# Performance work log

Measured on AMD Instinct MI355X. Metric: run time of the kernel, lower is better.

Reference implementation:

```python
import math
import jax, jax.numpy as jnp
import numpy as np

NUM_SUPERPIXELS = 256
COMPACTNESS = 10.0
NUM_ITERATIONS = 5


def _cdist(a, b):
    # Euclidean pairwise distance: a [B,N,C], b [B,K,C] -> [B,N,K]
    a2 = jnp.sum(a * a, axis=-1)[:, :, None]
    b2 = jnp.sum(b * b, axis=-1)[:, None, :]
    ab = jnp.einsum('bnc,bkc->bnk', a, b)
    return jnp.sqrt(jnp.maximum(a2 + b2 - 2.0 * ab, 1e-12))


def setup_inputs() -> dict:
    key = jax.random.key(0)
    x = jax.random.normal(key, (4, 200, 128, 128), dtype=jnp.float32)
    return {"x": x}


def reference(x):
    B, C, H, W = x.shape
    N = H * W

    # --- initialize_centers (grid of seed pixels, taken from x[0]) ---
    grid_h = int(math.sqrt(NUM_SUPERPIXELS * H / W))
    grid_w = NUM_SUPERPIXELS // grid_h
    K = grid_h * grid_w
    h_step, w_step = H // grid_h, W // grid_w
    h_idx = jnp.arange(h_step // 2, H, h_step)[:grid_h]
    w_idx = jnp.arange(w_step // 2, W, w_step)[:grid_w]
    gy, gx = jnp.meshgrid(h_idx, w_idx, indexing='ij')
    init_spatial = jnp.stack([gy.flatten(), gx.flatten()], axis=1).astype(jnp.float32)  # [K,2]
    flat_idx = gy.flatten() * W + gx.flatten()  # [K]

    # --- pixel coordinates ---
    yg, xg = jnp.meshgrid(jnp.arange(H), jnp.arange(W), indexing='ij')
    pix = jnp.stack([yg.flatten(), xg.flatten()], axis=1).astype(jnp.float32)  # [N,2]
    pix_b = jnp.broadcast_to(pix[None], (B, N, 2))

    x_flat = jnp.transpose(x, (0, 2, 3, 1)).reshape(B, N, C)  # [B,N,C]
    centers_spectral = jnp.broadcast_to(x_flat[0][flat_idx][None], (B, K, C))
    centers_spatial = jnp.broadcast_to(init_spatial[None], (B, K, 2))

    S = math.sqrt(H * W / NUM_SUPERPIXELS)
    Q = None
    for _ in range(NUM_ITERATIONS):
        D = _cdist(x_flat, centers_spectral) + (COMPACTNESS / S) * _cdist(pix_b, centers_spatial)
        Q = jax.nn.softmax(-D, axis=-1)  # [B,N,K]
        mass = jnp.sum(Q, axis=1)[:, :, None] + 1e-06  # [B,K,1]
        centers_spectral = jnp.einsum('bnk,bnc->bkc', Q, x_flat) / mass
        centers_spatial = jnp.einsum('bnk,bnc->bkc', Q, pix_b) / mass
    return Q, centers_spectral
```

## Files before the change

### kernel.cpp

```cpp
#include <hip/hip_runtime.h>
#include <math.h>

#define B 4
#define C 200
#define H 128
#define W 128
#define N 16384
#define K 256
#define ITERS 5
#define FACT 1.25f
#define NT 32
#define NTM 128
#define CPAD 208
#define CP2  224

typedef __attribute__((ext_vector_type(8))) __bf16 bf16x8;
typedef __attribute__((ext_vector_type(4))) __bf16 bf16x4;
typedef __attribute__((ext_vector_type(4))) float f32x4;

#define OFF_A2    0
#define OFF_CS    (OFF_A2 + B*N)
#define OFF_CSPAT (OFF_CS + B*K*C)
#define OFF_B2    (OFF_CSPAT + B*K*2)
#define OFF_SACC  (OFF_B2 + B*K)
#define OFF_MACC  (OFF_SACC + B*K*C)
#define OFF_SPACC (OFF_MACC + B*K)
#define OFF_CST   (OFF_SPACC + B*K*2)
#define CST_SZ    (B*C*K)
#define OFF_PART  (OFF_CST + CST_SZ)
#define PART_SZ   (B*NT*CPAD*K)
#define OFF_MPART (OFF_PART + PART_SZ)
#define MPART_SZ  (B*NTM*3*K)
#define WS_NEED   ((size_t)(OFF_MPART + MPART_SZ) * 4)
#define OFF_XBF   (OFF_MPART + MPART_SZ)
#define XBF_SZF   (B*N*CP2/2)
#define OFF_CSBF  (OFF_XBF + XBF_SZF)
#define CSBF_SZF  (B*K*CP2/2)
#define WS_NEED2  ((size_t)(OFF_CSBF + CSBF_SZF) * 4)
#define OFF_QTB   (OFF_CSBF + CSBF_SZF)
#define QTB_SZF   (B*K*N/2)
#define OFF_XB2   (OFF_QTB + QTB_SZF)
#define XB2_SZF   (B*CPAD*N/2)
#define WS_NEED3  ((size_t)(OFF_XB2 + XB2_SZF) * 4)

__global__ void k_init(const float* __restrict__ x, float* __restrict__ cs,
                       __bf16* __restrict__ csbf, float* __restrict__ cspat,
                       int fast) {
  int k = blockIdx.x, c = threadIdx.x;
  int i = k >> 4, j = k & 15;
  int sn = (4 + 8*i)*W + (4 + 8*j);
  if (c < C) {
    float v = x[(size_t)c*N + sn];
    for (int b = 0; b < B; ++b) {
      cs[((size_t)(b*K + k))*C + c] = v;
      if (fast) csbf[((size_t)(b*K + k))*CP2 + c] = (__bf16)v;
    }
  } else if (fast && c < CP2) {
    for (int b = 0; b < B; ++b)
      csbf[((size_t)(b*K + k))*CP2 + c] = (__bf16)0.f;
  }
  if (c == 0) {
    for (int b = 0; b < B; ++b) {
      cspat[(b*K + k)*2 + 0] = (float)(4 + 8*i);
      cspat[(b*K + k)*2 + 1] = (float)(4 + 8*j);
    }
  }
}

__global__ __launch_bounds__(256) void k_prep(const float* __restrict__ x,
                                              __bf16* __restrict__ xbf) {
  __shared__ float xt[32*64];
  int bid = blockIdx.x;
  int b  = bid >> 8;
  int n0 = (bid & 255) << 6;
  int tid = threadIdx.x;
  const float* xb = x + (size_t)b*C*N;
  __bf16* xo = xbf + ((size_t)b*N + n0)*CP2;
  for (int t = 0; t < 7; ++t) {
    int cc0 = t*32;
    __syncthreads();
    #pragma unroll
    for (int pass = 0; pass < 2; ++pass) {
      int f = pass*256 + tid;
      int ci = f >> 4, nq = f & 15;
      float4 v = make_float4(0.f, 0.f, 0.f, 0.f);
      if (cc0 + ci < C) v = *(const float4*)&xb[(size_t)(cc0 + ci)*N + n0 + nq*4];
      *(float4*)&xt[ci*64 + nq*4] = v;
    }
    __syncthreads();
    {
      int n = tid & 63, cg8 = (tid >> 6) * 8;
      bf16x8 pk;
      #pragma unroll
      for (int i = 0; i < 8; ++i) pk[i] = (__bf16)xt[(cg8 + i)*64 + n];
      *(bf16x8*)&xo[(size_t)n*CP2 + cc0 + cg8] = pk;
    }
  }
}

__global__ __launch_bounds__(256) void k_prep2(const float* __restrict__ x,
                                               __bf16* __restrict__ xbf2) {
  int g = blockIdx.x * 256 + threadIdx.x;
  int per_b = CPAD * (N/8);
  int b = g / per_b;
  int rem = g - b*per_b;
  int c = rem / (N/8);
  int n = (rem - c*(N/8)) * 8;
  bf16x8 pk;
  if (c < C) {
    const float* src = &x[((size_t)b*C + c)*N + n];
    float4 v0 = *(const float4*)&src[0];
    float4 v1 = *(const float4*)&src[4];
    pk[0]=(__bf16)v0.x; pk[1]=(__bf16)v0.y; pk[2]=(__bf16)v0.z; pk[3]=(__bf16)v0.w;
    pk[4]=(__bf16)v1.x; pk[5]=(__bf16)v1.y; pk[6]=(__bf16)v1.z; pk[7]=(__bf16)v1.w;
  } else {
    #pragma unroll
    for (int i = 0; i < 8; ++i) pk[i] = (__bf16)0.f;
  }
  *(bf16x8*)&xbf2[((size_t)b*CPAD + c)*N + n] = pk;
}

__global__ void k_a2(const float* __restrict__ x, float* __restrict__ a2) {
  int b = blockIdx.x >> 6;
  int n = ((blockIdx.x & 63) << 8) + threadIdx.x;
  const float* xp = x + (size_t)b*C*N + n;
  float s = 0.f;
  #pragma unroll 8
  for (int c = 0; c < C; ++c) { float v = xp[(size_t)c*N]; s += v*v; }
  a2[b*N + n] = s;
}

__global__ void k_b2(const float* __restrict__ cs, float* __restrict__ b2) {
  int bk = blockIdx.x;
  const float* p = cs + (size_t)bk*C;
  float s = 0.f;
  for (int c = threadIdx.x; c < C; c += 64) { float v = p[c]; s += v*v; }
  for (int off = 32; off > 0; off >>= 1) s += __shfl_down(s, off);
  if (threadIdx.x == 0) b2[bk] = s;
}

__global__ __launch_bounds__(512, 2) void k_assign2(
    const __bf16* __restrict__ xbf, const __bf16* __restrict__ csbf,
    const float* __restrict__ cspat, const float* __restrict__ b2,
    const float* __restrict__ a2, float* __restrict__ Q,
    __bf16* __restrict__ qtb, int wq) {
  __shared__ float b2s[K], cys[K], cxs[K];
  __shared__ float a2s[128];
  __shared__ float redw[8*128];
  __shared__ float redf[128];

  int b   = blockIdx.x >> 7;
  int n0  = (blockIdx.x & 127) << 7;
  int tid = threadIdx.x;
  int lane = tid & 63;
  int lr = lane & 15;
  int lg = lane >> 4;
  int w  = tid >> 6;

  if (tid < K) {
    b2s[tid] = b2[b*K + tid];
    cys[tid] = cspat[(b*K + tid)*2 + 0];
    cxs[tid] = cspat[(b*K + tid)*2 + 1];
  }
  if (tid < 128) a2s[tid] = a2[b*N + n0 + tid];
  __syncthreads();

  f32x4 acc[16];
  #pragma unroll
  for (int i = 0; i < 16; ++i) acc[i] = (f32x4){0.f, 0.f, 0.f, 0.f};

  const __bf16* cb = csbf + ((size_t)b*K + (size_t)(w*32 + lr))*CP2;
  const __bf16* xb = xbf + ((size_t)(b*N + n0 + lr))*CP2;

  for (int t = 0; t < 7; ++t) {
    int cc = t*32 + lg*8;
    bf16x8 b0 = *(const bf16x8*)&cb[cc];
    bf16x8 b1 = *(const bf16x8*)&cb[(size_t)16*CP2 + cc];
    #pragma unroll
    for (int nt = 0; nt < 8; ++nt) {
      bf16x8 av = *(const bf16x8*)&xb[(size_t)(nt*16)*CP2 + cc];
      acc[nt*2+0] = __builtin_amdgcn_mfma_f32_16x16x32_bf16(av, b0, acc[nt*2+0], 0, 0, 0);
      acc[nt*2+1] = __builtin_amdgcn_mfma_f32_16x16x32_bf16(av, b1, acc[nt*2+1], 0, 0, 0);
    }
  }

  float py = (float)(n0 >> 7);
  int k0 = w*32 + lr, k1 = k0 + 16;
  float b2v0 = b2s[k0], b2v1 = b2s[k1];
  float cx0 = cxs[k0], cx1 = cxs[k1];
  float dy0 = py - cys[k0], dy1 = py - cys[k1];
  float dyy0 = dy0*dy0, dyy1 = dy1*dy1;

  float mArr[32];
  #pragma unroll
  for (int nt = 0; nt < 8; ++nt) {
    #pragma unroll
    for (int r = 0; r < 4; ++r) {
      int pix = nt*16 + lg*4 + r;
      float a2v = a2s[pix];
      float pxv = (float)pix;
      float dx0 = pxv - cx0, dx1 = pxv - cx1;
      float d0 = sqrtf(fmaxf(a2v + b2v0 - 2.f*acc[nt*2+0][r], 1e-12f))
               + FACT*sqrtf(fmaxf(dyy0 + dx0*dx0, 1e-12f));
      float d1 = sqrtf(fmaxf(a2v + b2v1 - 2.f*acc[nt*2+1][r], 1e-12f))
               + FACT*sqrtf(fmaxf(dyy1 + dx1*dx1, 1e-12f));
      float e0 = __expf(-d0);
      float e1 = __expf(-d1);
      acc[nt*2+0][r] = e0;
      acc[nt*2+1][r] = e1;
      float s = e0 + e1;
      s += __shfl_xor(s, 1);
      s += __shfl_xor(s, 2);
      s += __shfl_xor(s, 4);
      s += __shfl_xor(s, 8);
      mArr[nt*4+r] = s;
    }
  }
  if (lr == 0) {
    #pragma unroll
    for (int nt = 0; nt < 8; ++nt)
      #pragma unroll
      for (int r = 0; r < 4; ++r)
        redw[w*128 + nt*16 + lg*4 + r] = mArr[nt*4+r];
  }
  __syncthreads();
  if (tid < 128) {
    float s = redw[tid];
    #pragma unroll
    for (int g = 1; g < 8; ++g) s += redw[g*128 + tid];
    redf[tid] = 1.f / s;
  }
  __syncthreads();
  float* Qb = Q + ((size_t)(b*N + n0))*K;
  __bf16* qt0 = qtb + ((size_t)b*K + k0)*N + n0;
  __bf16* qt1 = qtb + ((size_t)b*K + k1)*N + n0;
  #pragma unroll
  for (int nt = 0; nt < 8; ++nt) {
    bf16x4 p0, p1;
    #pragma unroll
    for (int r = 0; r < 4; ++r) {
      int pix = nt*16 + lg*4 + r;
      float inv = redf[pix];
      float f0 = acc[nt*2+0][r] * inv;
      float f1 = acc[nt*2+1][r] * inv;
      Qb[(size_t)pix*K + k0] = f0;
      Qb[(size_t)pix*K + k1] = f1;
      p0[r] = (__bf16)f0;
      p1[r] = (__bf16)f1;
    }
    if (wq) {
      *(bf16x4*)&qt0[nt*16 + lg*4] = p0;
      *(bf16x4*)&qt1[nt*16 + lg*4] = p1;
    }
  }
}

__global__ __launch_bounds__(512, 2) void k_assign(
    const float* __restrict__ x, const float* __restrict__ cs,
    const float* __restrict__ cspat, const float* __restrict__ b2,
    const float* __restrict__ a2, float* __restrict__ Q) {
  __shared__ __bf16 cs_lds[K*40];
  __shared__ __bf16 x_lds[128*40];
  __shared__ float b2s[K], cys[K], cxs[K];
  __shared__ float a2s[128];
  __shared__ float redw[8*128];
  __shared__ float redf[128];

  int b   = blockIdx.x >> 7;
  int n0  = (blockIdx.x & 127) << 7;
  int tid = threadIdx.x;
  int lane = tid & 63;
  int lr = lane & 15;
  int lg = lane >> 4;
  int w  = tid >> 6;

  if (tid < K) {
    b2s[tid] = b2[b*K + tid];
    cys[tid] = cspat[(b*K + tid)*2 + 0];
    cxs[tid] = cspat[(b*K + tid)*2 + 1];
  }
  if (tid < 128) a2s[tid] = a2[b*N + n0 + tid];

  f32x4 acc[16];
  #pragma unroll
  for (int i = 0; i < 16; ++i) acc[i] = (f32x4){0.f, 0.f, 0.f, 0.f};

  const float* xb = x + (size_t)b*C*N;
  const float* cb = cs + (size_t)b*K*C;

  for (int t = 0; t < 7; ++t) {
    int cc0 = t * 32;
    __syncthreads();
    #pragma unroll
    for (int pass = 0; pass < 4; ++pass) {
      int f = pass*512 + tid;
      int k = f >> 3, c4 = (f & 7) * 4;
      float4 v = make_float4(0.f, 0.f, 0.f, 0.f);
      if (cc0 + c4 < 200) v = *(const float4*)&cb[(size_t)k*C + cc0 + c4];
      __bf16* d = &cs_lds[k*40 + c4];
      d[0] = (__bf16)v.x; d[1] = (__bf16)v.y;
      d[2] = (__bf16)v.z; d[3] = (__bf16)v.w;
    }
    #pragma unroll
    for (int pass = 0; pass < 8; ++pass) {
      int idx = pass*512 + tid;
      int ci = idx >> 7, p = idx & 127;
      float xv = (cc0 + ci < 200) ? xb[(size_t)(cc0 + ci)*N + n0 + p] : 0.f;
      x_lds[p*40 + ci] = (__bf16)xv;
    }
    __syncthreads();
    const __bf16* bbase = &cs_lds[(w*32 + lr)*40 + lg*8];
    bf16x8 b0 = *(const bf16x8*)bbase;
    bf16x8 b1 = *(const bf16x8*)(bbase + 16*40);
    const __bf16* abase = &x_lds[lr*40 + lg*8];
    #pragma unroll
    for (int nt = 0; nt < 8; ++nt) {
      bf16x8 av = *(const bf16x8*)(abase + nt*16*40);
      acc[nt*2+0] = __builtin_amdgcn_mfma_f32_16x16x32_bf16(av, b0, acc[nt*2+0], 0, 0, 0);
      acc[nt*2+1] = __builtin_amdgcn_mfma_f32_16x16x32_bf16(av, b1, acc[nt*2+1], 0, 0, 0);
    }
  }

  float py = (float)(n0 >> 7);
  float mArr[32];
  #pragma unroll
  for (int nt = 0; nt < 8; ++nt) {
    #pragma unroll
    for (int r = 0; r < 4; ++r) {
      int pix = nt*16 + lg*4 + r;
      float a2v = a2s[pix];
      float pxv = (float)pix;
      float dmin = 1e30f;
      #pragma unroll
      for (int j = 0; j < 2; ++j) {
        int k = w*32 + j*16 + lr;
        float ab = acc[nt*2+j][r];
        float dy = py - cys[k];
        float dx = pxv - cxs[k];
        float d = sqrtf(fmaxf(a2v + b2s[k] - 2.f*ab, 1e-12f))
                + FACT*sqrtf(fmaxf(dy*dy + dx*dx, 1e-12f));
        acc[nt*2+j][r] = d;
        dmin = fminf(dmin, d);
      }
      mArr[nt*4+r] = dmin;
    }
  }
  #pragma unroll
  for (int i = 0; i < 32; ++i) {
    float m = mArr[i];
    m = fminf(m, __shfl_xor(m, 1));
    m = fminf(m, __shfl_xor(m, 2));
    m = fminf(m, __shfl_xor(m, 4));
    m = fminf(m, __shfl_xor(m, 8));
    mArr[i] = m;
  }
  if (lr == 0) {
    #pragma unroll
    for (int nt = 0; nt < 8; ++nt)
      #pragma unroll
      for (int r = 0; r < 4; ++r)
        redw[w*128 + nt*16 + lg*4 + r] = mArr[nt*4+r];
  }
  __syncthreads();
  if (tid < 128) {
    float m = redw[tid];
    #pragma unroll
    for (int g = 1; g < 8; ++g) m = fminf(m, redw[g*128 + tid]);
    redf[tid] = m;
  }
  __syncthreads();
  #pragma unroll
  for (int nt = 0; nt < 8; ++nt) {
    #pragma unroll
    for (int r = 0; r < 4; ++r) {
      int pix = nt*16 + lg*4 + r;
      float mnv = redf[pix];
      float s = 0.f;
      #pragma unroll
      for (int j = 0; j < 2; ++j) {
        float e = __expf(mnv - acc[nt*2+j][r]);
        acc[nt*2+j][r] = e;
        s += e;
      }
      s += __shfl_xor(s, 1);
      s += __shfl_xor(s, 2);
      s += __shfl_xor(s, 4);
      s += __shfl_xor(s, 8);
      mArr[nt*4+r] = s;
    }
  }
  if (lr == 0) {
    #pragma unroll
    for (int nt = 0; nt < 8; ++nt)
      #pragma unroll
      for (int r = 0; r < 4; ++r)
        redw[w*128 + nt*16 + lg*4 + r] = mArr[nt*4+r];
  }
  __syncthreads();
  if (tid < 128) {
    float s = redw[tid];
    #pragma unroll
    for (int g = 1; g < 8; ++g) s += redw[g*128 + tid];
    redf[tid] = 1.f / s;
  }
  __syncthreads();
  float* Qb = Q + ((size_t)(b*N + n0))*K;
  #pragma unroll
  for (int nt = 0; nt < 8; ++nt) {
    #pragma unroll
    for (int r = 0; r < 4; ++r) {
      int pix = nt*16 + lg*4 + r;
      float inv = redf[pix];
      #pragma unroll
      for (int j = 0; j < 2; ++j) {
        int k = w*32 + j*16 + lr;
        Qb[(size_t)pix*K + k] = acc[nt*2+j][r] * inv;
      }
    }
  }
}

__global__ __launch_bounds__(256) void k_update5(
    const __bf16* __restrict__ qtb, const __bf16* __restrict__ xbf2,
    float* __restrict__ part) {
  int bid = blockIdx.x;
  int b   = bid >> 7;
  int rem = bid & 127;
  int cg  = rem >> 5;
  int nt  = rem & 31;
  int tid = threadIdx.x;
  int lane = tid & 63, lr = lane & 15, lg = lane >> 4;
  int w   = tid >> 6;
  int c0  = cg * 64;

  f32x4 acc[16];
  #pragma unroll
  for (int i = 0; i < 16; ++i) acc[i] = (f32x4){0.f, 0.f, 0.f, 0.f};

  const __bf16* qb = qtb + ((size_t)b*K + (size_t)(w*64 + lr))*N;
  int cr0 = c0 + lr;
  int cr1 = min(c0 + 16 + lr, CPAD - 1);
  int cr2 = min(c0 + 32 + lr, CPAD - 1);
  int cr3 = min(c0 + 48 + lr, CPAD - 1);
  const __bf16* xb0 = xbf2 + ((size_t)b*CPAD + cr0)*N;
  const __bf16* xb1 = xbf2 + ((size_t)b*CPAD + cr1)*N;
  const __bf16* xb2 = xbf2 + ((size_t)b*CPAD + cr2)*N;
  const __bf16* xb3 = xbf2 + ((size_t)b*CPAD + cr3)*N;

  for (int ch = 0; ch < 16; ++ch) {
    int nb = nt*512 + ch*32 + lg*8;
    bf16x8 A0 = *(const bf16x8*)&qb[nb];
    bf16x8 A1 = *(const bf16x8*)&qb[(size_t)16*N + nb];
    bf16x8 A2 = *(const bf16x8*)&qb[(size_t)32*N + nb];
    bf16x8 A3 = *(const bf16x8*)&qb[(size_t)48*N + nb];
    bf16x8 B0 = *(const bf16x8*)&xb0[nb];
    bf16x8 B1 = *(const bf16x8*)&xb1[nb];
    bf16x8 B2 = *(const bf16x8*)&xb2[nb];
    bf16x8 B3 = *(const bf16x8*)&xb3[nb];
    acc[0]  = __builtin_amdgcn_mfma_f32_16x16x32_bf16(A0, B0, acc[0], 0, 0, 0);
    acc[1]  = __builtin_amdgcn_mfma_f32_16x16x32_bf16(A0, B1, acc[1], 0, 0, 0);
    acc[2]  = __builtin_amdgcn_mfma_f32_16x16x32_bf16(A0, B2, acc[2], 0, 0, 0);
    acc[3]  = __builtin_amdgcn_mfma_f32_16x16x32_bf16(A0, B3, acc[3], 0, 0, 0);
    acc[4]  = __builtin_amdgcn_mfma_f32_16x16x32_bf16(A1, B0, acc[4], 0, 0, 0);
    acc[5]  = __builtin_amdgcn_mfma_f32_16x16x32_bf16(A1, B1, acc[5], 0, 0, 0);
    acc[6]  = __builtin_amdgcn_mfma_f32_16x16x32_bf16(A1, B2, acc[6], 0, 0, 0);
    acc[7]  = __builtin_amdgcn_mfma_f32_16x16x32_bf16(A1, B3, acc[7], 0, 0, 0);
    acc[8]  = __builtin_amdgcn_mfma_f32_16x16x32_bf16(A2, B0, acc[8], 0, 0, 0);
    acc[9]  = __builtin_amdgcn_mfma_f32_16x16x32_bf16(A2, B1, acc[9], 0, 0, 0);
    acc[10] = __builtin_amdgcn_mfma_f32_16x16x32_bf16(A2, B2, acc[10], 0, 0, 0);
    acc[11] = __builtin_amdgcn_mfma_f32_16x16x32_bf16(A2, B3, acc[11], 0, 0, 0);
    acc[12] = __builtin_amdgcn_mfma_f32_16x16x32_bf16(A3, B0, acc[12], 0, 0, 0);
    acc[13] = __builtin_amdgcn_mfma_f32_16x16x32_bf16(A3, B1, acc[13], 0, 0, 0);
    acc[14] = __builtin_amdgcn_mfma_f32_16x16x32_bf16(A3, B2, acc[14], 0, 0, 0);
    acc[15] = __builtin_amdgcn_mfma_f32_16x16x32_bf16(A3, B3, acc[15], 0, 0, 0);
  }

  float* pp = part + (size_t)(b*NT + nt) * CPAD * K;
  #pragma unroll
  for (int t = 0; t < 4; ++t) {
    #pragma unroll
    for (int u = 0; u < 4; ++u) {
      int c = c0 + u*16 + lr;
      if (c < CPAD) {
        int k = w*64 + t*16 + lg*4;
        *(f32x4*)&pp[(size_t)c*K + k] = acc[t*4+u];
      }
    }
  }
}

__global__ __launch_bounds__(256) void k_update4(
    const float* __restrict__ x, const float* __restrict__ Q,
    float* __restrict__ part) {
  __shared__ float  q32[32*256];
  __shared__ __bf16 qbf[256*40];
  __shared__ __bf16 xbf[64*40];
  int bid = blockIdx.x;
  int b   = bid >> 7;
  int rem = bid & 127;
  int cg  = rem >> 5;
  int nt  = rem & 31;
  int tid = threadIdx.x;
  int lane = tid & 63, lr = lane & 15, lg = lane >> 4;
  int w   = tid >> 6;
  int c0  = cg * 64;

  f32x4 acc[16];
  #pragma unroll
  for (int i = 0; i < 16; ++i) acc[i] = (f32x4){0.f, 0.f, 0.f, 0.f};

  const float* Qb = Q + (size_t)b*N*K;
  const float* xb = x + (size_t)b*C*N;

  for (int ch = 0; ch < 16; ++ch) {
    int nb = nt*512 + ch*32;
    __syncthreads();
    #pragma unroll
    for (int pass = 0; pass < 8; ++pass) {
      int f = pass*256 + tid;
      int n = f >> 6, k4 = f & 63;
      *(float4*)&q32[n*256 + k4*4] =
          *(const float4*)&Qb[(size_t)(nb + n)*K + k4*4];
    }
    #pragma unroll
    for (int pass = 0; pass < 2; ++pass) {
      int f = pass*256 + tid;
      int c = f >> 3, n4 = f & 7;
      int cc = c0 + c;
      float4 v = make_float4(0.f, 0.f, 0.f, 0.f);
      if (cc < 200) v = *(const float4*)&xb[(size_t)cc*N + nb + n4*4];
      __bf16* d = &xbf[c*40 + n4*4];
      d[0] = (__bf16)v.x; d[1] = (__bf16)v.y;
      d[2] = (__bf16)v.z; d[3] = (__bf16)v.w;
    }
    __syncthreads();
    {
      #pragma unroll
      for (int g = 0; g < 4; ++g) {
        bf16x8 pk;
        #pragma unroll
        for (int i = 0; i < 8; ++i)
          pk[i] = (__bf16)q32[(g*8 + i)*256 + tid];
        *(bf16x8*)&qbf[tid*40 + g*8] = pk;
      }
    }
    __syncthreads();
    const __bf16* abase = &qbf[(w*64 + lr)*40 + lg*8];
    const __bf16* bbase = &xbf[lr*40 + lg*8];
    bf16x8 A0 = *(const bf16x8*)(abase);
    bf16x8 A1 = *(const bf16x8*)(abase + 16*40);
    bf16x8 A2 = *(const bf16x8*)(abase + 32*40);
    bf16x8 A3 = *(const bf16x8*)(abase + 48*40);
    bf16x8 B0 = *(const bf16x8*)(bbase);
    bf16x8 B1 = *(const bf16x8*)(bbase + 16*40);
    bf16x8 B2 = *(const bf16x8*)(bbase + 32*40);
    bf16x8 B3 = *(const bf16x8*)(bbase + 48*40);
    acc[0]  = __builtin_amdgcn_mfma_f32_16x16x32_bf16(A0, B0, acc[0], 0, 0, 0);
    acc[1]  = __builtin_amdgcn_mfma_f32_16x16x32_bf16(A0, B1, acc[1], 0, 0, 0);
    acc[2]  = __builtin_amdgcn_mfma_f32_16x16x32_bf16(A0, B2, acc[2], 0, 0, 0);
    acc[3]  = __builtin_amdgcn_mfma_f32_16x16x32_bf16(A0, B3, acc[3], 0, 0, 0);
    acc[4]  = __builtin_amdgcn_mfma_f32_16x16x32_bf16(A1, B0, acc[4], 0, 0, 0);
    acc[5]  = __builtin_amdgcn_mfma_f32_16x16x32_bf16(A1, B1, acc[5], 0, 0, 0);
    acc[6]  = __builtin_amdgcn_mfma_f32_16x16x32_bf16(A1, B2, acc[6], 0, 0, 0);
    acc[7]  = __builtin_amdgcn_mfma_f32_16x16x32_bf16(A1, B3, acc[7], 0, 0, 0);
    acc[8]  = __builtin_amdgcn_mfma_f32_16x16x32_bf16(A2, B0, acc[8], 0, 0, 0);
    acc[9]  = __builtin_amdgcn_mfma_f32_16x16x32_bf16(A2, B1, acc[9], 0, 0, 0);
    acc[10] = __builtin_amdgcn_mfma_f32_16x16x32_bf16(A2, B2, acc[10], 0, 0, 0);
    acc[11] = __builtin_amdgcn_mfma_f32_16x16x32_bf16(A2, B3, acc[11], 0, 0, 0);
    acc[12] = __builtin_amdgcn_mfma_f32_16x16x32_bf16(A3, B0, acc[12], 0, 0, 0);
    acc[13] = __builtin_amdgcn_mfma_f32_16x16x32_bf16(A3, B1, acc[13], 0, 0, 0);
    acc[14] = __builtin_amdgcn_mfma_f32_16x16x32_bf16(A3, B2, acc[14], 0, 0, 0);
    acc[15] = __builtin_amdgcn_mfma_f32_16x16x32_bf16(A3, B3, acc[15], 0, 0, 0);
  }

  float* pp = part + (size_t)(b*NT + nt) * CPAD * K;
  #pragma unroll
  for (int t = 0; t < 4; ++t) {
    #pragma unroll
    for (int u = 0; u < 4; ++u) {
      int c = c0 + u*16 + lr;
      if (c < CPAD) {
        int k = w*64 + t*16 + lg*4;
        *(f32x4*)&pp[(size_t)c*K + k] = acc[t*4+u];
      }
    }
  }
}

__global__ __launch_bounds__(256) void k_mass(
    const float* __restrict__ Q, float* __restrict__ mpart) {
  int bid = blockIdx.x;
  int b = bid >> 7, nt = bid & 127;
  int tid = threadIdx.x;
  const float* Qb = Q + (size_t)b*N*K;
  int nbase = nt * 128;
  float mass = 0.f, sy = 0.f, sx = 0.f;
  for (int nn = 0; nn < 128; nn += 8) {
    float qv[8];
    #pragma unroll
    for (int j = 0; j < 8; ++j)
      qv[j] = Qb[(size_t)(nbase + nn + j)*K + tid];
    #pragma unroll
    for (int j = 0; j < 8; ++j) {
      int n = nbase + nn + j;
      mass += qv[j];
      sy += qv[j] * (float)(n >> 7);
      sx += qv[j] * (float)(n & 127);
    }
  }
  float* mp = mpart + (size_t)(b*NTM + nt) * 3 * K;
  mp[tid]       = mass;
  mp[K + tid]   = sy;
  mp[2*K + tid] = sx;
}

__global__ __launch_bounds__(256) void k_reduce(
    const float* __restrict__ part, const float* __restrict__ mpart,
    float* __restrict__ sacc, float* __restrict__ macc,
    float* __restrict__ spacc) {
  int bid = blockIdx.x;
  int b = bid / 200;
  int c = bid % 200;
  int tid = threadIdx.x;
  float s = 0.f;
  for (int nt = 0; nt < NT; ++nt)
    s += part[((size_t)(b*NT + nt)*CPAD + c)*K + tid];
  sacc[(size_t)(b*K + tid)*C + c] = s;
  if (c == 0) {
    float m = 0.f, yy = 0.f, xx = 0.f;
    for (int nt = 0; nt < NTM; ++nt) {
      const float* mp = mpart + (size_t)(b*NTM + nt) * 3 * K;
      m  += mp[tid];
      yy += mp[K + tid];
      xx += mp[2*K + tid];
    }
    macc[b*K + tid] = m;
    spacc[(b*K + tid)*2 + 0] = yy;
    spacc[(b*K + tid)*2 + 1] = xx;
  }
}

__global__ __launch_bounds__(256, 2) void k_update(
    const float* __restrict__ x, const float* __restrict__ Q,
    float* __restrict__ sacc, float* __restrict__ macc,
    float* __restrict__ spacc) {
  __shared__ float x_lds[32*28];
  int bid = blockIdx.x;
  int b = bid >> 9;
  int rest = bid & 511;
  int ct = rest >> 6;
  int nt = rest & 63;
  int tid = threadIdx.x;
  int c0 = ct * 25;

  float acc[25];
  #pragma unroll
  for (int c = 0; c < 25; ++c) acc[c] = 0.f;
  float mass = 0.f, sy = 0.f, sx = 0.f;

  const float* xb = x + (size_t)b*C*N + (size_t)c0*N;
  const float* Qb = Q + (size_t)b*N*K;

  for (int ch = 0; ch < 8; ++ch) {
    int nb = nt*256 + ch*32;
    __syncthreads();
    #pragma unroll
    for (int pass = 0; pass < 4; ++pass) {
      int idx = pass*256 + tid;
      if (idx < 800) {
        int ci = idx >> 5, nn = idx & 31;
        x_lds[nn*28 + ci] = xb[(size_t)ci*N + nb + nn];
      }
    }
    __syncthreads();
    float py  = (float)(nb >> 7);
    float pxb = (float)(nb & 127);
    #pragma unroll
    for (int n4 = 0; n4 < 8; ++n4) {
      float qv[4];
      #pragma unroll
      for (int j = 0; j < 4; ++j)
        qv[j] = Qb[(size_t)(nb + n4*4 + j)*K + tid];
      #pragma unroll
      for (int j = 0; j < 4; ++j) {
        int nn = n4*4 + j;
        float q = qv[j];
        if (ct == 0) {
          mass += q;
          sy += q * py;
          sx += q * (pxb + (float)nn);
        }
        const float* xr = &x_lds[nn*28];
        #pragma unroll
        for (int c4 = 0; c4 < 6; ++c4) {
          float4 xv = *(const float4*)&xr[c4*4];
          acc[c4*4+0] = fmaf(q, xv.x, acc[c4*4+0]);
          acc[c4*4+1] = fmaf(q, xv.y, acc[c4*4+1]);
          acc[c4*4+2] = fmaf(q, xv.z, acc[c4*4+2]);
          acc[c4*4+3] = fmaf(q, xv.w, acc[c4*4+3]);
        }
        acc[24] = fmaf(q, xr[24], acc[24]);
      }
    }
  }
  float* sp = sacc + ((size_t)(b*K + tid))*C + c0;
  #pragma unroll
  for (int c = 0; c < 25; ++c) atomicAdd(&sp[c], acc[c]);
  if (ct == 0) {
    atomicAdd(&macc[b*K + tid], mass);
    atomicAdd(&spacc[(b*K + tid)*2 + 0], sy);
    atomicAdd(&spacc[(b*K + tid)*2 + 1], sx);
  }
}

__global__ void k_final(const float* __restrict__ sacc, const float* __restrict__ macc,
                        const float* __restrict__ spacc, float* __restrict__ cs,
                        __bf16* __restrict__ csbf, float* __restrict__ cspat,
                        float* __restrict__ b2, float* __restrict__ outc,
                        int last, int fast) {
  __shared__ float red[256];
  int bk = blockIdx.x;
  int c = threadIdx.x;
  float inv = 1.f / (macc[bk] + 1e-6f);
  float v = 0.f;
  if (c < C) {
    v = sacc[(size_t)bk*C + c] * inv;
    cs[(size_t)bk*C + c] = v;
    if (fast) csbf[(size_t)bk*CP2 + c] = (__bf16)v;
    if (last) outc[(size_t)bk*C + c] = v;
  } else if (c == C) {
    cspat[bk*2 + 0] = spacc[bk*2 + 0] * inv;
  } else if (c == C + 1) {
    cspat[bk*2 + 1] = spacc[bk*2 + 1] * inv;
  }
  red[c] = v * v;
  __syncthreads();
  for (int off = 128; off > 0; off >>= 1) {
    if (c < off) red[c] += red[c + off];
    __syncthreads();
  }
  if (c == 0) b2[bk] = red[0];
}

extern "C" void kernel_launch(void* const* d_in, const int* in_sizes, int n_in,
                              void* d_out, int out_size, void* d_ws, size_t ws_size,
                              hipStream_t stream) {
  const float* x = (const float*)d_in[0];
  float* out = (float*)d_out;
  float* ws  = (float*)d_ws;
  float* a2    = ws + OFF_A2;
  float* cs    = ws + OFF_CS;
  float* cspat = ws + OFF_CSPAT;
  float* b2    = ws + OFF_B2;
  float* sacc  = ws + OFF_SACC;
  float* macc  = ws + OFF_MACC;
  float* spacc = ws + OFF_SPACC;
  float* part  = ws + OFF_PART;
  float* mpart = ws + OFF_MPART;
  __bf16* xbf  = (__bf16*)(ws + OFF_XBF);
  __bf16* csbf = (__bf16*)(ws + OFF_CSBF);
  __bf16* qtb  = (__bf16*)(ws + OFF_QTB);
  __bf16* xbf2 = (__bf16*)(ws + OFF_XB2);
  float* outc  = out + (size_t)B*N*K;
  int split = (ws_size >= WS_NEED) ? 1 : 0;
  int fast  = (ws_size >= WS_NEED2) ? 1 : 0;
  int fast2 = (ws_size >= WS_NEED3) ? 1 : 0;

  hipLaunchKernelGGL(k_init, dim3(K), dim3(256), 0, stream, x, cs, csbf, cspat, fast);
  hipLaunchKernelGGL(k_a2, dim3(B*64), dim3(256), 0, stream, x, a2);
  hipLaunchKernelGGL(k_b2, dim3(B*K), dim3(64), 0, stream, cs, b2);
  if (fast)
    hipLaunchKernelGGL(k_prep, dim3(B*256), dim3(256), 0, stream, x, xbf);
  if (fast2)
    hipLaunchKernelGGL(k_prep2, dim3(B*CPAD*N/8/256), dim3(256), 0, stream, x, xbf2);
  for (int it = 0; it < ITERS; ++it) {
    if (fast)
      hipLaunchKernelGGL(k_assign2, dim3(B*128), dim3(512), 0, stream,
                         xbf, csbf, cspat, b2, a2, out, qtb, fast2);
    else
      hipLaunchKernelGGL(k_assign, dim3(B*128), dim3(512), 0, stream,
                         x, cs, cspat, b2, a2, out);
    if (split) {
      if (fast2)
        hipLaunchKernelGGL(k_update5, dim3(B*4*NT), dim3(256), 0, stream,
                           qtb, xbf2, part);
      else
        hipLaunchKernelGGL(k_update4, dim3(B*4*NT), dim3(256), 0, stream,
                           x, out, part);
      hipLaunchKernelGGL(k_mass, dim3(B*NTM), dim3(256), 0, stream,
                         out, mpart);
      hipLaunchKernelGGL(k_reduce, dim3(B*200), dim3(256), 0, stream,
                         part, mpart, sacc, macc, spacc);
    } else {
      hipMemsetAsync(sacc, 0, (size_t)(B*K*C + B*K + B*K*2)*sizeof(float), stream);
      hipLaunchKernelGGL(k_update, dim3(B*512), dim3(256), 0, stream,
                         x, out, sacc, macc, spacc);
    }
    hipLaunchKernelGGL(k_final, dim3(B*K), dim3(256), 0, stream,
                       sacc, macc, spacc, cs, csbf, cspat, b2, outc,
                       (it == ITERS-1) ? 1 : 0, fast);
  }
}
```

Measured before the change: 646.7 us.

## Fold mass and spatial sums into GEMM padding rows, skip intermediate Q writes

```diff
diff --git a/kernel.cpp b/kernel.cpp
--- a/kernel.cpp
+++ b/kernel.cpp
@@ -113,6 +113,16 @@
     float4 v1 = *(const float4*)&src[4];
     pk[0]=(__bf16)v0.x; pk[1]=(__bf16)v0.y; pk[2]=(__bf16)v0.z; pk[3]=(__bf16)v0.w;
     pk[4]=(__bf16)v1.x; pk[5]=(__bf16)v1.y; pk[6]=(__bf16)v1.z; pk[7]=(__bf16)v1.w;
+  } else if (c == 200) {
+    #pragma unroll
+    for (int i = 0; i < 8; ++i) pk[i] = (__bf16)1.0f;
+  } else if (c == 201) {
+    float py = (float)(n >> 7);
+    #pragma unroll
+    for (int i = 0; i < 8; ++i) pk[i] = (__bf16)py;
+  } else if (c == 202) {
+    #pragma unroll
+    for (int i = 0; i < 8; ++i) pk[i] = (__bf16)(float)((n & 127) + i);
   } else {
     #pragma unroll
     for (int i = 0; i < 8; ++i) pk[i] = (__bf16)0.f;
@@ -143,7 +153,7 @@
     const __bf16* __restrict__ xbf, const __bf16* __restrict__ csbf,
     const float* __restrict__ cspat, const float* __restrict__ b2,
     const float* __restrict__ a2, float* __restrict__ Q,
-    __bf16* __restrict__ qtb, int wq) {
+    __bf16* __restrict__ qtb, int wq, int wout) {
   __shared__ float b2s[K], cys[K], cxs[K];
   __shared__ float a2s[128];
   __shared__ float redw[8*128];
@@ -243,8 +253,10 @@
       float inv = redf[pix];
       float f0 = acc[nt*2+0][r] * inv;
       float f1 = acc[nt*2+1][r] * inv;
-      Qb[(size_t)pix*K + k0] = f0;
-      Qb[(size_t)pix*K + k1] = f1;
+      if (wout) {
+        Qb[(size_t)pix*K + k0] = f0;
+        Qb[(size_t)pix*K + k1] = f1;
+      }
       p0[r] = (__bf16)f0;
       p1[r] = (__bf16)f1;
     }
@@ -617,7 +629,7 @@
 __global__ __launch_bounds__(256) void k_reduce(
     const float* __restrict__ part, const float* __restrict__ mpart,
     float* __restrict__ sacc, float* __restrict__ macc,
-    float* __restrict__ spacc) {
+    float* __restrict__ spacc, int fast2) {
   int bid = blockIdx.x;
   int b = bid / 200;
   int c = bid % 200;
@@ -628,11 +640,20 @@
   sacc[(size_t)(b*K + tid)*C + c] = s;
   if (c == 0) {
     float m = 0.f, yy = 0.f, xx = 0.f;
-    for (int nt = 0; nt < NTM; ++nt) {
-      const float* mp = mpart + (size_t)(b*NTM + nt) * 3 * K;
-      m  += mp[tid];
-      yy += mp[K + tid];
-      xx += mp[2*K + tid];
+    if (fast2) {
+      for (int nt = 0; nt < NT; ++nt) {
+        const float* pb = part + (size_t)(b*NT + nt)*CPAD*K;
+        m  += pb[(size_t)200*K + tid];
+        yy += pb[(size_t)201*K + tid];
+        xx += pb[(size_t)202*K + tid];
+      }
+    } else {
+      for (int nt = 0; nt < NTM; ++nt) {
+        const float* mp = mpart + (size_t)(b*NTM + nt) * 3 * K;
+        m  += mp[tid];
+        yy += mp[K + tid];
+        xx += mp[2*K + tid];
+      }
     }
     macc[b*K + tid] = m;
     spacc[(b*K + tid)*2 + 0] = yy;
@@ -774,23 +795,26 @@
   if (fast2)
     hipLaunchKernelGGL(k_prep2, dim3(B*CPAD*N/8/256), dim3(256), 0, stream, x, xbf2);
   for (int it = 0; it < ITERS; ++it) {
+    int last = (it == ITERS-1) ? 1 : 0;
+    int wout = (!fast2 || last) ? 1 : 0;
     if (fast)
       hipLaunchKernelGGL(k_assign2, dim3(B*128), dim3(512), 0, stream,
-                         xbf, csbf, cspat, b2, a2, out, qtb, fast2);
+                         xbf, csbf, cspat, b2, a2, out, qtb, fast2, wout);
     else
       hipLaunchKernelGGL(k_assign, dim3(B*128), dim3(512), 0, stream,
                          x, cs, cspat, b2, a2, out);
     if (split) {
-      if (fast2)
+      if (fast2) {
         hipLaunchKernelGGL(k_update5, dim3(B*4*NT), dim3(256), 0, stream,
                            qtb, xbf2, part);
-      else
+      } else {
         hipLaunchKernelGGL(k_update4, dim3(B*4*NT), dim3(256), 0, stream,
                            x, out, part);
-      hipLaunchKernelGGL(k_mass, dim3(B*NTM), dim3(256), 0, stream,
-                         out, mpart);
+        hipLaunchKernelGGL(k_mass, dim3(B*NTM), dim3(256), 0, stream,
+                           out, mpart);
+      }
       hipLaunchKernelGGL(k_reduce, dim3(B*200), dim3(256), 0, stream,
-                         part, mpart, sacc, macc, spacc);
+                         part, mpart, sacc, macc, spacc, fast2);
     } else {
       hipMemsetAsync(sacc, 0, (size_t)(B*K*C + B*K + B*K*2)*sizeof(float), stream);
       hipLaunchKernelGGL(k_update, dim3(B*512), dim3(256), 0, stream,
@@ -798,6 +822,6 @@
     }
     hipLaunchKernelGGL(k_final, dim3(B*K), dim3(256), 0, stream,
                        sacc, macc, spacc, cs, csbf, cspat, b2, outc,
-                       (it == ITERS-1) ? 1 : 0, fast);
-  }
-}
+                       last, fast);
+  }
+}
```

Result: faster. 539.1 us, median of 2 (-16.6%).
